# Kernel optimization log

Measured on AMD Instinct MI355X. Metric: run time of the kernel, lower is better.

The kernel has to match this reference:

```python
import jax, jax.numpy as jnp
import numpy as np

N = 100000
E = 1280000
D = 64


def setup_inputs() -> dict:
    key = jax.random.key(0)
    k1, k2, k3, k4, k5, k6 = jax.random.split(key, 6)
    return {
        "x": jax.random.normal(k1, (N, D), dtype=jnp.float32),
        "w_src": jax.random.normal(k2, (D,), dtype=jnp.float32),
        "w_dst": jax.random.normal(k3, (D,), dtype=jnp.float32),
        "ew": jax.random.normal(k4, (E,), dtype=jnp.float32),
        "src_idx": jax.random.randint(k5, (E,), 0, N, dtype=jnp.int64),
        "dst_idx": jax.random.randint(k6, (E,), 0, N, dtype=jnp.int64),
    }


def reference(x, w_src, w_dst, ew, src_idx, dst_idx):
    # Per-node scalar scores: Linear(emb_dim, 1, bias=False)
    a_src = x @ w_src            # [N]
    a_dst = x @ w_dst            # [N]
    # Edge attention: tanh(a_src[u] + a_dst[v]) * ew  (u_add_v + tanh + scale)
    a = jnp.tanh(a_src[src_idx] + a_dst[dst_idx]) * ew   # [E]
    # Message = a_e * x[src_e]; reduce = scatter-sum over dst (u_mul_e + sum)
    m = a[:, None] * x[src_idx]                           # [E, D]
    h = jax.ops.segment_sum(m, dst_idx, num_segments=N)   # [N, D]
    return h
```

## Files before the change

### kernel.cpp

```cpp
#include <hip/hip_runtime.h>
#include <hip/hip_fp16.h>
#include <math.h>

#define DIM  64
#define SPAN 256
#define SPAN_SHIFT 8
#define NBIN 256
#define KMAX 512
#define CAP  6144

__global__ void score_kernel(const float* __restrict__ x,
                             const float* __restrict__ w_src,
                             const float* __restrict__ w_dst,
                             float* __restrict__ a_src,
                             float* __restrict__ a_dst,
                             __half* __restrict__ xh,
                             int N) {
    int gid  = blockIdx.x * blockDim.x + threadIdx.x;
    int node = gid >> 6;
    int lane = threadIdx.x & 63;
    if (node >= N) return;
    float xv = x[(size_t)node * DIM + lane];
    xh[(size_t)node * DIM + lane] = __float2half_rn(xv);
    float s1 = xv * w_src[lane];
    float s2 = xv * w_dst[lane];
    #pragma unroll
    for (int off = 32; off > 0; off >>= 1) {
        s1 += __shfl_down(s1, off, 64);
        s2 += __shfl_down(s2, off, 64);
    }
    if (lane == 0) {
        a_src[node] = s1;
        a_dst[node] = s2;
    }
}

__global__ __launch_bounds__(1024) void hist_coarse(
        const int* __restrict__ dst, int* __restrict__ cnt,
        int E, int N, int K) {
    __shared__ int lh[KMAX];
    int tid = threadIdx.x;
    for (int j = tid; j < K; j += blockDim.x) lh[j] = 0;
    __syncthreads();
    for (int base = blockIdx.x * 2048; base < E; base += NBIN * 2048) {
        int e = base + (tid << 1);
        if (e + 1 < E) {
            int2 t2 = *(const int2*)(dst + e);
            unsigned t0 = (unsigned)t2.x; if (t0 >= (unsigned)N) t0 = 0;
            unsigned t1 = (unsigned)t2.y; if (t1 >= (unsigned)N) t1 = 0;
            atomicAdd(&lh[t0 >> SPAN_SHIFT], 1);
            atomicAdd(&lh[t1 >> SPAN_SHIFT], 1);
        } else if (e < E) {
            unsigned t = (unsigned)dst[e];
            if (t >= (unsigned)N) t = 0;
            atomicAdd(&lh[t >> SPAN_SHIFT], 1);
        }
    }
    __syncthreads();
    for (int j = tid; j < K; j += blockDim.x)
        cnt[j * NBIN + blockIdx.x] = lh[j];
}

__global__ void scan_part(const int* __restrict__ cnt, int* __restrict__ offs,
                          int* __restrict__ bsum, int N) {
    __shared__ int buf[2][256];
    int tid = threadIdx.x;
    int i = blockIdx.x * 256 + tid;
    int v = (i < N) ? cnt[i] : 0;
    int sel = 0;
    buf[0][tid] = v;
    __syncthreads();
    for (int off = 1; off < 256; off <<= 1) {
        int nsel = sel ^ 1;
        buf[nsel][tid] = buf[sel][tid] + ((tid >= off) ? buf[sel][tid - off] : 0);
        __syncthreads();
        sel = nsel;
    }
    if (i < N) offs[i] = buf[sel][tid] - v;
    if (tid == 255) bsum[blockIdx.x] = buf[sel][255];
}

__global__ void scan_top(int* __restrict__ bsum, int* __restrict__ offs,
                         int NB, int N) {
    __shared__ int buf[2][512];
    int tid = threadIdx.x;
    int v = (tid < NB) ? bsum[tid] : 0;
    int sel = 0;
    buf[0][tid] = v;
    __syncthreads();
    for (int off = 1; off < 512; off <<= 1) {
        int nsel = sel ^ 1;
        buf[nsel][tid] = buf[sel][tid] + ((tid >= off) ? buf[sel][tid - off] : 0);
        __syncthreads();
        sel = nsel;
    }
    if (tid < NB) bsum[tid] = buf[sel][tid] - v;
    if (tid == 511) offs[N] = buf[sel][511];
}

__global__ __launch_bounds__(1024) void binpass_kernel(
        const float* __restrict__ ew,
        const int* __restrict__ src_idx,
        const int* __restrict__ dst_idx,
        const float* __restrict__ a_src,
        const float* __restrict__ a_dst,
        const int* __restrict__ moffs,
        const int* __restrict__ bsum,
        unsigned long long* __restrict__ pay,
        int E, int N, int K) {
    __shared__ int lcur[KMAX];
    int tid = threadIdx.x;
    for (int j = tid; j < K; j += blockDim.x) {
        int i = j * NBIN + blockIdx.x;
        lcur[j] = moffs[i] + bsum[i >> 8];
    }
    __syncthreads();
    for (int base = blockIdx.x * 2048; base < E; base += NBIN * 2048) {
        int e = base + (tid << 1);
        if (e + 1 < E) {
            int2   s2 = *(const int2*)(src_idx + e);
            int2   t2 = *(const int2*)(dst_idx + e);
            float2 w2 = *(const float2*)(ew + e);
            unsigned s0 = (unsigned)s2.x; if (s0 >= (unsigned)N) s0 = 0;
            unsigned t0 = (unsigned)t2.x; if (t0 >= (unsigned)N) t0 = 0;
            unsigned s1 = (unsigned)s2.y; if (s1 >= (unsigned)N) s1 = 0;
            unsigned t1 = (unsigned)t2.y; if (t1 >= (unsigned)N) t1 = 0;
            float a0 = tanhf(a_src[s0] + a_dst[t0]) * w2.x;
            float a1 = tanhf(a_src[s1] + a_dst[t1]) * w2.y;
            int p0 = atomicAdd(&lcur[t0 >> SPAN_SHIFT], 1);
            int p1 = atomicAdd(&lcur[t1 >> SPAN_SHIFT], 1);
            unsigned r0 = (s0 << 8) | (t0 & (SPAN - 1u));
            unsigned r1 = (s1 << 8) | (t1 & (SPAN - 1u));
            pay[p0] = ((unsigned long long)r0 << 32) |
                      (unsigned long long)__float_as_uint(a0);
            pay[p1] = ((unsigned long long)r1 << 32) |
                      (unsigned long long)__float_as_uint(a1);
        } else if (e < E) {
            unsigned s = (unsigned)src_idx[e];
            unsigned t = (unsigned)dst_idx[e];
            if (s >= (unsigned)N) s = 0;
            if (t >= (unsigned)N) t = 0;
            float a = tanhf(a_src[s] + a_dst[t]) * ew[e];
            int pos = atomicAdd(&lcur[t >> SPAN_SHIFT], 1);
            unsigned rec = (s << 8) | (t & (SPAN - 1u));
            pay[pos] = ((unsigned long long)rec << 32) |
                       (unsigned long long)__float_as_uint(a);
        }
    }
}

__global__ __launch_bounds__(1024) void sort_gather_kernel(
        const __half* __restrict__ xh,
        const float* __restrict__ x32,
        const unsigned long long* __restrict__ pay,
        const int* __restrict__ moffs,
        const int* __restrict__ bsum,
        float* __restrict__ h,
        int N, int K, int E) {
    __shared__ unsigned long long srec[CAP];
    __shared__ unsigned short sidx[CAP];
    __shared__ int hcnt[SPAN];
    __shared__ int hoff[2][SPAN];
    __shared__ int lcur[SPAN];
    __shared__ int nstart[SPAN];
    int tid = threadIdx.x;
    int b   = blockIdx.x;
    int i0 = b * NBIN;
    int bstart = moffs[i0] + bsum[i0 >> 8];
    int bend;
    if (b == K - 1) bend = E;
    else { int i1 = (b + 1) * NBIN; bend = moffs[i1] + bsum[i1 >> 8]; }
    int cnt = bend - bstart;

    if (cnt <= CAP) {
        if (tid < SPAN) hcnt[tid] = 0;
        __syncthreads();
        for (int i = tid; i < cnt; i += 1024) {
            unsigned long long r = pay[bstart + i];
            srec[i] = r;
            atomicAdd(&hcnt[(int)((r >> 32) & (SPAN - 1u))], 1);
        }
        __syncthreads();
        int sel = 0;
        if (tid < SPAN) hoff[0][tid] = hcnt[tid];
        __syncthreads();
        for (int off = 1; off < SPAN; off <<= 1) {
            int nsel = sel ^ 1;
            if (tid < SPAN)
                hoff[nsel][tid] = hoff[sel][tid] +
                                  ((tid >= off) ? hoff[sel][tid - off] : 0);
            __syncthreads();
            sel = nsel;
        }
        if (tid < SPAN) {
            int excl = hoff[sel][tid] - hcnt[tid];
            nstart[tid] = excl;
            lcur[tid]   = excl;
        }
        __syncthreads();
        for (int i = tid; i < cnt; i += 1024) {
            unsigned long long r = srec[i];
            int d = (int)((r >> 32) & (SPAN - 1u));
            int pos = atomicAdd(&lcur[d], 1);
            sidx[pos] = (unsigned short)i;
        }
        __syncthreads();
        int lane = tid & 63;
        int wave = tid >> 6;
        int grp  = lane >> 4;
        int sub  = lane & 15;
        for (int d = wave; d < SPAN; d += 16) {
            int node = b * SPAN + d;
            if (node >= N) break;
            int p  = nstart[d];
            int pe = p + hcnt[d];
            float ax = 0.f, ay = 0.f, az = 0.f, aw = 0.f;
            while (p + 8 <= pe) {
                unsigned long long r0 = srec[sidx[p + grp]];
                unsigned long long r1 = srec[sidx[p + 4 + grp]];
                p += 8;
                unsigned s0 = (unsigned)(r0 >> 40); if (s0 >= (unsigned)N) s0 = 0;
                unsigned s1 = (unsigned)(r1 >> 40); if (s1 >= (unsigned)N) s1 = 0;
                uint2 v0 = *(const uint2*)(xh + (size_t)s0 * DIM + (sub << 2));
                uint2 v1 = *(const uint2*)(xh + (size_t)s1 * DIM + (sub << 2));
                float a0 = __uint_as_float((unsigned)r0);
                float a1 = __uint_as_float((unsigned)r1);
                float2 l0 = __half22float2(*(const __half2*)&v0.x);
                float2 h0 = __half22float2(*(const __half2*)&v0.y);
                float2 l1 = __half22float2(*(const __half2*)&v1.x);
                float2 h1 = __half22float2(*(const __half2*)&v1.y);
                ax = fmaf(a0, l0.x, ax); ay = fmaf(a0, l0.y, ay);
                az = fmaf(a0, h0.x, az); aw = fmaf(a0, h0.y, aw);
                ax = fmaf(a1, l1.x, ax); ay = fmaf(a1, l1.y, ay);
                az = fmaf(a1, h1.x, az); aw = fmaf(a1, h1.y, aw);
            }
            while (p < pe) {
                int q = p + grp;
                float a0 = 0.f;
                unsigned s0 = 0;
                if (q < pe) {
                    unsigned long long r0 = srec[sidx[q]];
                    a0 = __uint_as_float((unsigned)r0);
                    s0 = (unsigned)(r0 >> 40); if (s0 >= (unsigned)N) s0 = 0;
                }
                p += 4;
                uint2 v0 = *(const uint2*)(xh + (size_t)s0 * DIM + (sub << 2));
                float2 l0 = __half22float2(*(const __half2*)&v0.x);
                float2 h0 = __half22float2(*(const __half2*)&v0.y);
                ax = fmaf(a0, l0.x, ax); ay = fmaf(a0, l0.y, ay);
                az = fmaf(a0, h0.x, az); aw = fmaf(a0, h0.y, aw);
            }
            ax += __shfl_xor(ax, 16, 64); ay += __shfl_xor(ay, 16, 64);
            az += __shfl_xor(az, 16, 64); aw += __shfl_xor(aw, 16, 64);
            ax += __shfl_xor(ax, 32, 64); ay += __shfl_xor(ay, 32, 64);
            az += __shfl_xor(az, 32, 64); aw += __shfl_xor(aw, 32, 64);
            if (grp == 0) {
                float4 out = make_float4(ax, ay, az, aw);
                *(float4*)(h + (size_t)node * DIM + (sub << 2)) = out;
            }
        }
    } else {
        for (int j = tid; j < SPAN * DIM; j += 1024) {
            int node = b * SPAN + (j >> 6);
            if (node < N) h[(size_t)node * DIM + (j & 63)] = 0.f;
        }
        __syncthreads();
        for (int i = tid; i < cnt; i += 1024) {
            unsigned long long r = pay[bstart + i];
            unsigned s = (unsigned)(r >> 40);
            if (s >= (unsigned)N) s = 0;
            int node = b * SPAN + (int)((r >> 32) & (SPAN - 1u));
            float a = __uint_as_float((unsigned)r);
            if (node < N)
                for (int k = 0; k < DIM; ++k)
                    atomicAdd(&h[(size_t)node * DIM + k],
                              a * x32[(size_t)s * DIM + k]);
        }
    }
}

__global__ void zero_h_kernel(float* __restrict__ p, int n) {
    int i = blockIdx.x * blockDim.x + threadIdx.x;
    if (i < n) p[i] = 0.f;
}

__global__ void edge_kernel_atomic(const float* __restrict__ x,
                                   const float* __restrict__ ew,
                                   const int* __restrict__ src_idx,
                                   const int* __restrict__ dst_idx,
                                   const float* __restrict__ a_src,
                                   const float* __restrict__ a_dst,
                                   float* __restrict__ h,
                                   int E) {
    int gid  = blockIdx.x * blockDim.x + threadIdx.x;
    int e    = gid >> 6;
    int lane = threadIdx.x & 63;
    if (e >= E) return;
    int s = src_idx[e];
    int t = dst_idx[e];
    float a  = tanhf(a_src[s] + a_dst[t]) * ew[e];
    float xv = x[(size_t)s * DIM + lane];
    atomicAdd(&h[(size_t)t * DIM + lane], a * xv);
}

__global__ void score_only_kernel(const float* __restrict__ x,
                                  const float* __restrict__ w_src,
                                  const float* __restrict__ w_dst,
                                  float* __restrict__ a_src,
                                  float* __restrict__ a_dst,
                                  int N) {
    int gid  = blockIdx.x * blockDim.x + threadIdx.x;
    int node = gid >> 6;
    int lane = threadIdx.x & 63;
    if (node >= N) return;
    float xv = x[(size_t)node * DIM + lane];
    float s1 = xv * w_src[lane];
    float s2 = xv * w_dst[lane];
    #pragma unroll
    for (int off = 32; off > 0; off >>= 1) {
        s1 += __shfl_down(s1, off, 64);
        s2 += __shfl_down(s2, off, 64);
    }
    if (lane == 0) {
        a_src[node] = s1;
        a_dst[node] = s2;
    }
}

extern "C" void kernel_launch(void* const* d_in, const int* in_sizes, int n_in,
                              void* d_out, int out_size, void* d_ws, size_t ws_size,
                              hipStream_t stream) {
    const float* x     = (const float*)d_in[0];
    const float* w_src = (const float*)d_in[1];
    const float* w_dst = (const float*)d_in[2];
    const float* ew    = (const float*)d_in[3];
    const int*   src   = (const int*)d_in[4];
    const int*   dst   = (const int*)d_in[5];
    float* h = (float*)d_out;

    int N = in_sizes[0] / DIM;
    int E = in_sizes[3];

    int K    = (N + SPAN - 1) / SPAN;
    int Ntot = K * NBIN;
    int NBs  = (Ntot + 255) / 256;

    float* a_src  = (float*)d_ws;
    float* a_dst  = a_src + N;
    int*   moffs  = (int*)(a_dst + N);
    int*   bsum   = moffs + Ntot + 1;
    size_t head_bytes = ((size_t)(2 * N) + (size_t)Ntot + 1 + (size_t)NBs) * 4;
    size_t pay_off = (head_bytes + 15) & ~(size_t)15;
    unsigned long long* pay = (unsigned long long*)((char*)d_ws + pay_off);
    size_t xh_off = pay_off + (size_t)E * 8;
    __half* xh = (__half*)((char*)d_ws + xh_off);
    size_t need = xh_off + (size_t)N * DIM * 2;

    int score_blocks = (N + 3) / 4;

    if (ws_size < need || K > KMAX || NBs > 512 || (N * DIM) % 2 != 0) {
        score_only_kernel<<<score_blocks, 256, 0, stream>>>(x, w_src, w_dst,
                                                            a_src, a_dst, N);
        int ob = (out_size + 255) / 256;
        zero_h_kernel<<<ob, 256, 0, stream>>>(h, out_size);
        int edge_blocks = (E + 3) / 4;
        edge_kernel_atomic<<<edge_blocks, 256, 0, stream>>>(x, ew, src, dst,
                                                            a_src, a_dst, h, E);
        return;
    }

    score_kernel<<<score_blocks, 256, 0, stream>>>(x, w_src, w_dst,
                                                   a_src, a_dst, xh, N);
    hist_coarse<<<NBIN, 1024, 0, stream>>>(dst, moffs, E, N, K);
    scan_part<<<NBs, 256, 0, stream>>>(moffs, moffs, bsum, Ntot);
    scan_top<<<1, 512, 0, stream>>>(bsum, moffs, NBs, Ntot);
    binpass_kernel<<<NBIN, 1024, 0, stream>>>(ew, src, dst, a_src, a_dst,
                                              moffs, bsum, pay, E, N, K);
    sort_gather_kernel<<<K, 1024, 0, stream>>>(xh, x, pay, moffs, bsum,
                                               h, N, K, E);
}
```

Measured before the change: 174.2 us.

## Fuse score and histogram kernels, fold top-level scan into binpass

Merges the per-node score/fp16-conversion kernel with the coarse destination histogram in one launch: the first 256 blocks also build histograms, and scores now use float4 loads across 16 lanes per node. The single-block top-level scan is removed. Every binpass block recomputes the 512-entry block-sum scan in shared memory, and block 0 writes a per-bucket base array that sort_gather reads directly. This removes two launches and their serialization gaps, at the cost of redundant scan work per binpass block and load imbalance in the fused kernel, where 256 blocks carry the histogram loop.

```diff
diff --git a/kernel.cpp b/kernel.cpp
--- a/kernel.cpp
+++ b/kernel.cpp
@@ -1,6 +1,8 @@
 #include <hip/hip_runtime.h>
 #include <hip/hip_fp16.h>
 #include <math.h>
+
+typedef unsigned long long ull;
 
 #define DIM  64
 #define SPAN 256
@@ -9,56 +11,68 @@
 #define KMAX 512
 #define CAP  6144
 
-__global__ void score_kernel(const float* __restrict__ x,
-                             const float* __restrict__ w_src,
-                             const float* __restrict__ w_dst,
-                             float* __restrict__ a_src,
-                             float* __restrict__ a_dst,
-                             __half* __restrict__ xh,
-                             int N) {
-    int gid  = blockIdx.x * blockDim.x + threadIdx.x;
-    int node = gid >> 6;
-    int lane = threadIdx.x & 63;
-    if (node >= N) return;
-    float xv = x[(size_t)node * DIM + lane];
-    xh[(size_t)node * DIM + lane] = __float2half_rn(xv);
-    float s1 = xv * w_src[lane];
-    float s2 = xv * w_dst[lane];
-    #pragma unroll
-    for (int off = 32; off > 0; off >>= 1) {
-        s1 += __shfl_down(s1, off, 64);
-        s2 += __shfl_down(s2, off, 64);
-    }
-    if (lane == 0) {
-        a_src[node] = s1;
-        a_dst[node] = s2;
-    }
-}
-
-__global__ __launch_bounds__(1024) void hist_coarse(
-        const int* __restrict__ dst, int* __restrict__ cnt,
-        int E, int N, int K) {
+__global__ __launch_bounds__(256) void score_hist_kernel(
+        const float* __restrict__ x,
+        const float* __restrict__ w_src,
+        const float* __restrict__ w_dst,
+        const int* __restrict__ dst_idx,
+        float* __restrict__ a_src,
+        float* __restrict__ a_dst,
+        __half* __restrict__ xh,
+        int* __restrict__ cnt,
+        int N, int E, int K) {
     __shared__ int lh[KMAX];
     int tid = threadIdx.x;
-    for (int j = tid; j < K; j += blockDim.x) lh[j] = 0;
-    __syncthreads();
-    for (int base = blockIdx.x * 2048; base < E; base += NBIN * 2048) {
-        int e = base + (tid << 1);
-        if (e + 1 < E) {
-            int2 t2 = *(const int2*)(dst + e);
-            unsigned t0 = (unsigned)t2.x; if (t0 >= (unsigned)N) t0 = 0;
-            unsigned t1 = (unsigned)t2.y; if (t1 >= (unsigned)N) t1 = 0;
-            atomicAdd(&lh[t0 >> SPAN_SHIFT], 1);
-            atomicAdd(&lh[t1 >> SPAN_SHIFT], 1);
-        } else if (e < E) {
-            unsigned t = (unsigned)dst[e];
-            if (t >= (unsigned)N) t = 0;
-            atomicAdd(&lh[t >> SPAN_SHIFT], 1);
-        }
-    }
-    __syncthreads();
-    for (int j = tid; j < K; j += blockDim.x)
-        cnt[j * NBIN + blockIdx.x] = lh[j];
+    int b   = blockIdx.x;
+    bool histblk = (b < NBIN);
+    if (histblk) {
+        for (int j = tid; j < K; j += 256) lh[j] = 0;
+        __syncthreads();
+    }
+    int lane = tid & 63;
+    int wave = tid >> 6;
+    int grp  = lane >> 4;
+    int sub  = lane & 15;
+    int node = b * 16 + wave * 4 + grp;
+    if (node < N) {
+        float4 v  = ((const float4*)x)[(size_t)node * 16 + sub];
+        float4 ws = ((const float4*)w_src)[sub];
+        float4 wd = ((const float4*)w_dst)[sub];
+        float s1 = v.x * ws.x + v.y * ws.y + v.z * ws.z + v.w * ws.w;
+        float s2 = v.x * wd.x + v.y * wd.y + v.z * wd.z + v.w * wd.w;
+        #pragma unroll
+        for (int off = 1; off < 16; off <<= 1) {
+            s1 += __shfl_xor(s1, off, 64);
+            s2 += __shfl_xor(s2, off, 64);
+        }
+        if (sub == 0) { a_src[node] = s1; a_dst[node] = s2; }
+        __half2 h01 = __floats2half2_rn(v.x, v.y);
+        __half2 h23 = __floats2half2_rn(v.z, v.w);
+        uint2 hv;
+        hv.x = *(unsigned*)&h01;
+        hv.y = *(unsigned*)&h23;
+        *(uint2*)(xh + (size_t)node * DIM + (sub << 2)) = hv;
+    }
+    if (histblk) {
+        for (int base = b * 2048; base < E; base += NBIN * 2048) {
+            for (int off = tid << 1; off < 2048; off += 512) {
+                int e = base + off;
+                if (e + 1 < E) {
+                    int2 t2 = *(const int2*)(dst_idx + e);
+                    unsigned t0 = (unsigned)t2.x; if (t0 >= (unsigned)N) t0 = 0;
+                    unsigned t1 = (unsigned)t2.y; if (t1 >= (unsigned)N) t1 = 0;
+                    atomicAdd(&lh[t0 >> SPAN_SHIFT], 1);
+                    atomicAdd(&lh[t1 >> SPAN_SHIFT], 1);
+                } else if (e < E) {
+                    unsigned t = (unsigned)dst_idx[e];
+                    if (t >= (unsigned)N) t = 0;
+                    atomicAdd(&lh[t >> SPAN_SHIFT], 1);
+                }
+            }
+        }
+        __syncthreads();
+        for (int j = tid; j < K; j += 256) cnt[j * NBIN + b] = lh[j];
+    }
 }
 
 __global__ void scan_part(const int* __restrict__ cnt, int* __restrict__ offs,
@@ -80,24 +94,6 @@
     if (tid == 255) bsum[blockIdx.x] = buf[sel][255];
 }
 
-__global__ void scan_top(int* __restrict__ bsum, int* __restrict__ offs,
-                         int NB, int N) {
-    __shared__ int buf[2][512];
-    int tid = threadIdx.x;
-    int v = (tid < NB) ? bsum[tid] : 0;
-    int sel = 0;
-    buf[0][tid] = v;
-    __syncthreads();
-    for (int off = 1; off < 512; off <<= 1) {
-        int nsel = sel ^ 1;
-        buf[nsel][tid] = buf[sel][tid] + ((tid >= off) ? buf[sel][tid - off] : 0);
-        __syncthreads();
-        sel = nsel;
-    }
-    if (tid < NB) bsum[tid] = buf[sel][tid] - v;
-    if (tid == 511) offs[N] = buf[sel][511];
-}
-
 __global__ __launch_bounds__(1024) void binpass_kernel(
         const float* __restrict__ ew,
         const int* __restrict__ src_idx,
@@ -106,16 +102,38 @@
         const float* __restrict__ a_dst,
         const int* __restrict__ moffs,
         const int* __restrict__ bsum,
-        unsigned long long* __restrict__ pay,
-        int E, int N, int K) {
+        int* __restrict__ gbase,
+        ull* __restrict__ pay,
+        int E, int N, int K, int NBs) {
     __shared__ int lcur[KMAX];
+    __shared__ int buf[2][512];
     int tid = threadIdx.x;
-    for (int j = tid; j < K; j += blockDim.x) {
-        int i = j * NBIN + blockIdx.x;
-        lcur[j] = moffs[i] + bsum[i >> 8];
+    int b   = blockIdx.x;
+    int v = 0;
+    if (tid < 512) {
+        v = (tid < NBs) ? bsum[tid] : 0;
+        buf[0][tid] = v;
     }
     __syncthreads();
-    for (int base = blockIdx.x * 2048; base < E; base += NBIN * 2048) {
+    int sel = 0;
+    for (int off = 1; off < 512; off <<= 1) {
+        if (tid < 512)
+            buf[sel ^ 1][tid] = buf[sel][tid] +
+                                ((tid >= off) ? buf[sel][tid - off] : 0);
+        __syncthreads();
+        sel ^= 1;
+    }
+    int esel = sel ^ 1;
+    if (tid < 512) buf[esel][tid] = buf[sel][tid] - v;
+    __syncthreads();
+    if (b == 0 && tid < 512) {
+        if (tid < NBs) gbase[tid] = buf[esel][tid];
+        if (tid == NBs) gbase[NBs] = E;
+    }
+    for (int j = tid; j < K; j += 1024)
+        lcur[j] = moffs[j * NBIN + b] + buf[esel][j];
+    __syncthreads();
+    for (int base = b * 2048; base < E; base += NBIN * 2048) {
         int e = base + (tid << 1);
         if (e + 1 < E) {
             int2   s2 = *(const int2*)(src_idx + e);
@@ -131,10 +149,8 @@
             int p1 = atomicAdd(&lcur[t1 >> SPAN_SHIFT], 1);
             unsigned r0 = (s0 << 8) | (t0 & (SPAN - 1u));
             unsigned r1 = (s1 << 8) | (t1 & (SPAN - 1u));
-            pay[p0] = ((unsigned long long)r0 << 32) |
-                      (unsigned long long)__float_as_uint(a0);
-            pay[p1] = ((unsigned long long)r1 << 32) |
-                      (unsigned long long)__float_as_uint(a1);
+            pay[p0] = ((ull)r0 << 32) | (ull)__float_as_uint(a0);
+            pay[p1] = ((ull)r1 << 32) | (ull)__float_as_uint(a1);
         } else if (e < E) {
             unsigned s = (unsigned)src_idx[e];
             unsigned t = (unsigned)dst_idx[e];
@@ -143,8 +159,7 @@
             float a = tanhf(a_src[s] + a_dst[t]) * ew[e];
             int pos = atomicAdd(&lcur[t >> SPAN_SHIFT], 1);
             unsigned rec = (s << 8) | (t & (SPAN - 1u));
-            pay[pos] = ((unsigned long long)rec << 32) |
-                       (unsigned long long)__float_as_uint(a);
+            pay[pos] = ((ull)rec << 32) | (ull)__float_as_uint(a);
         }
     }
 }
@@ -152,12 +167,11 @@
 __global__ __launch_bounds__(1024) void sort_gather_kernel(
         const __half* __restrict__ xh,
         const float* __restrict__ x32,
-        const unsigned long long* __restrict__ pay,
-        const int* __restrict__ moffs,
-        const int* __restrict__ bsum,
+        const ull* __restrict__ pay,
+        const int* __restrict__ gbase,
         float* __restrict__ h,
         int N, int K, int E) {
-    __shared__ unsigned long long srec[CAP];
+    __shared__ ull srec[CAP];
     __shared__ unsigned short sidx[CAP];
     __shared__ int hcnt[SPAN];
     __shared__ int hoff[2][SPAN];
@@ -165,18 +179,15 @@
     __shared__ int nstart[SPAN];
     int tid = threadIdx.x;
     int b   = blockIdx.x;
-    int i0 = b * NBIN;
-    int bstart = moffs[i0] + bsum[i0 >> 8];
-    int bend;
-    if (b == K - 1) bend = E;
-    else { int i1 = (b + 1) * NBIN; bend = moffs[i1] + bsum[i1 >> 8]; }
+    int bstart = gbase[b];
+    int bend   = gbase[b + 1];
     int cnt = bend - bstart;
 
     if (cnt <= CAP) {
         if (tid < SPAN) hcnt[tid] = 0;
         __syncthreads();
         for (int i = tid; i < cnt; i += 1024) {
-            unsigned long long r = pay[bstart + i];
+            ull r = pay[bstart + i];
             srec[i] = r;
             atomicAdd(&hcnt[(int)((r >> 32) & (SPAN - 1u))], 1);
         }
@@ -199,7 +210,7 @@
         }
         __syncthreads();
         for (int i = tid; i < cnt; i += 1024) {
-            unsigned long long r = srec[i];
+            ull r = srec[i];
             int d = (int)((r >> 32) & (SPAN - 1u));
             int pos = atomicAdd(&lcur[d], 1);
             sidx[pos] = (unsigned short)i;
@@ -216,8 +227,8 @@
             int pe = p + hcnt[d];
             float ax = 0.f, ay = 0.f, az = 0.f, aw = 0.f;
             while (p + 8 <= pe) {
-                unsigned long long r0 = srec[sidx[p + grp]];
-                unsigned long long r1 = srec[sidx[p + 4 + grp]];
+                ull r0 = srec[sidx[p + grp]];
+                ull r1 = srec[sidx[p + 4 + grp]];
                 p += 8;
                 unsigned s0 = (unsigned)(r0 >> 40); if (s0 >= (unsigned)N) s0 = 0;
                 unsigned s1 = (unsigned)(r1 >> 40); if (s1 >= (unsigned)N) s1 = 0;
@@ -239,7 +250,7 @@
                 float a0 = 0.f;
                 unsigned s0 = 0;
                 if (q < pe) {
-                    unsigned long long r0 = srec[sidx[q]];
+                    ull r0 = srec[sidx[q]];
                     a0 = __uint_as_float((unsigned)r0);
                     s0 = (unsigned)(r0 >> 40); if (s0 >= (unsigned)N) s0 = 0;
                 }
@@ -266,7 +277,7 @@
         }
         __syncthreads();
         for (int i = tid; i < cnt; i += 1024) {
-            unsigned long long r = pay[bstart + i];
+            ull r = pay[bstart + i];
             unsigned s = (unsigned)(r >> 40);
             if (s >= (unsigned)N) s = 0;
             int node = b * SPAN + (int)((r >> 32) & (SPAN - 1u));
@@ -344,21 +355,24 @@
     int K    = (N + SPAN - 1) / SPAN;
     int Ntot = K * NBIN;
     int NBs  = (Ntot + 255) / 256;
+    int sh_blocks = (N + 15) / 16;
 
     float* a_src  = (float*)d_ws;
     float* a_dst  = a_src + N;
     int*   moffs  = (int*)(a_dst + N);
     int*   bsum   = moffs + Ntot + 1;
-    size_t head_bytes = ((size_t)(2 * N) + (size_t)Ntot + 1 + (size_t)NBs) * 4;
+    int*   gbase  = bsum + NBs;
+    size_t head_bytes = ((size_t)(2 * N) + (size_t)Ntot + 1 + (size_t)NBs +
+                         (size_t)(K + 1)) * 4;
     size_t pay_off = (head_bytes + 15) & ~(size_t)15;
-    unsigned long long* pay = (unsigned long long*)((char*)d_ws + pay_off);
+    ull* pay = (ull*)((char*)d_ws + pay_off);
     size_t xh_off = pay_off + (size_t)E * 8;
     __half* xh = (__half*)((char*)d_ws + xh_off);
     size_t need = xh_off + (size_t)N * DIM * 2;
 
-    int score_blocks = (N + 3) / 4;
-
-    if (ws_size < need || K > KMAX || NBs > 512 || (N * DIM) % 2 != 0) {
+    if (ws_size < need || K > KMAX || K < 1 || NBs != K || NBs > 512 ||
+        sh_blocks < NBIN || (N * DIM) % 2 != 0) {
+        int score_blocks = (N + 3) / 4;
         score_only_kernel<<<score_blocks, 256, 0, stream>>>(x, w_src, w_dst,
                                                             a_src, a_dst, N);
         int ob = (out_size + 255) / 256;
@@ -369,13 +383,13 @@
         return;
     }
 
-    score_kernel<<<score_blocks, 256, 0, stream>>>(x, w_src, w_dst,
-                                                   a_src, a_dst, xh, N);
-    hist_coarse<<<NBIN, 1024, 0, stream>>>(dst, moffs, E, N, K);
+    score_hist_kernel<<<sh_blocks, 256, 0, stream>>>(x, w_src, w_dst, dst,
+                                                     a_src, a_dst, xh, moffs,
+                                                     N, E, K);
     scan_part<<<NBs, 256, 0, stream>>>(moffs, moffs, bsum, Ntot);
-    scan_top<<<1, 512, 0, stream>>>(bsum, moffs, NBs, Ntot);
     binpass_kernel<<<NBIN, 1024, 0, stream>>>(ew, src, dst, a_src, a_dst,
-                                              moffs, bsum, pay, E, N, K);
-    sort_gather_kernel<<<K, 1024, 0, stream>>>(xh, x, pay, moffs, bsum,
+                                              moffs, bsum, gbase, pay,
+                                              E, N, K, NBs);
+    sort_gather_kernel<<<K, 1024, 0, stream>>>(xh, x, pay, gbase,
                                                h, N, K, E);
 }
```

Result: faster. 166.0 us (median of 2 runs) (-4.7%).
